# Optimization experiments

Measured on AMD Instinct MI355X. Metric: run time of the kernel, lower is better.

Reference implementation:

```python
import jax, jax.numpy as jnp
import numpy as np

B, P, S = 128, 10, 8
L, BF = 81, 75
OF, MF2 = 40, 20
C = 64
H = 3 * C  # hidden_size = 192
NCHAR = 8
EPS = 1e-5


def setup_inputs() -> dict:
    key = jax.random.key(0)
    ks = jax.random.split(key, 24)
    n = lambda i, shp: jax.random.normal(ks[i], shp, jnp.float32)
    w = lambda i, shp: jax.random.normal(ks[i], shp, jnp.float32) * 0.02
    return {
        "board": n(0, (B, P, S, L, BF)),
        "order": n(1, (B, P, S, OF)),
        "message": n(2, (B, P, S, MF2)),
        "other_ind": jax.random.uniform(ks[3], (B, P, 7), jnp.float32),
        "me_ind": jax.random.uniform(ks[4], (B, P, 7), jnp.float32),
        "h0": n(5, (P, B, H)),
        "c0": n(6, (P, B, H)),
        "Wb1": w(7, (1024, L * BF)), "bb1": jnp.zeros((1024,), jnp.float32),
        "Wb2": w(8, (256, 1024)), "bb2": jnp.zeros((256,), jnp.float32),
        "Wb3": w(9, (C, 256)), "bb3": jnp.zeros((C,), jnp.float32),
        "Wo1": w(10, (128, OF)), "bo1": jnp.zeros((128,), jnp.float32),
        "Wo2": w(11, (32, 128)), "bo2": jnp.zeros((32,), jnp.float32),
        "Wo3": w(12, (C, 32)), "bo3": jnp.zeros((C,), jnp.float32),
        "Wm1": w(13, (64, MF2)), "bm1": jnp.zeros((64,), jnp.float32),
        "Wm2": w(14, (32, 64)), "bm2": jnp.zeros((32,), jnp.float32),
        "Wm3": w(15, (C, 32)), "bm3": jnp.zeros((C,), jnp.float32),
        "g1": jnp.ones((C,), jnp.float32), "be1": jnp.zeros((C,), jnp.float32),
        "g2": jnp.ones((C,), jnp.float32), "be2": jnp.zeros((C,), jnp.float32),
        "g3": jnp.ones((C,), jnp.float32), "be3": jnp.zeros((C,), jnp.float32),
        "Wih": w(16, (4 * H, H)), "Whh": w(17, (4 * H, H)),
        "bih": jnp.zeros((4 * H,), jnp.float32), "bhh": jnp.zeros((4 * H,), jnp.float32),
        "Wf1": w(18, (256, S * H)), "bf1": jnp.zeros((256,), jnp.float32),
        "Wf2": w(19, (NCHAR, 256 + 14)), "bf2": jnp.zeros((NCHAR,), jnp.float32),
    }


def _mlp3(x, W1, b1, W2, b2, W3, b3):
    x = jax.nn.relu(x @ W1.T + b1)
    x = jax.nn.relu(x @ W2.T + b2)
    return x @ W3.T + b3


def _bn_relu(x, g, b):
    # x: [b, C, S]; BatchNorm1d in training mode -> biased batch stats over (N, L)
    m = x.mean(axis=(0, 2), keepdims=True)
    v = jnp.mean((x - m) ** 2, axis=(0, 2), keepdims=True)
    return jax.nn.relu(g[None, :, None] * (x - m) * jax.lax.rsqrt(v + EPS) + b[None, :, None])


def _forward(board, order, message, other_ind, me_ind, h0, c0,
             Wb1, bb1, Wb2, bb2, Wb3, bb3, Wo1, bo1, Wo2, bo2, Wo3, bo3,
             Wm1, bm1, Wm2, bm2, Wm3, bm3, g1, be1, g2, be2, g3, be3,
             Wih, Whh, bih, bhh, Wf1, bf1, Wf2, bf2):
    num_step = board.shape[2]

    def per_past(board_p, order_p, msg_p, oi_p, mi_p, h, c):
        bb = board_p.shape[0]
        bf = _mlp3(board_p.reshape(bb * num_step, -1), Wb1, bb1, Wb2, bb2, Wb3, bb3)
        bf = _bn_relu(jnp.swapaxes(bf.reshape(bb, num_step, -1), 1, 2), g1, be1)
        of = _mlp3(order_p.reshape(bb * num_step, -1), Wo1, bo1, Wo2, bo2, Wo3, bo3)
        of = _bn_relu(jnp.swapaxes(of.reshape(bb, num_step, -1), 1, 2), g2, be2)
        mf = _mlp3(msg_p.reshape(bb * num_step, -1), Wm1, bm1, Wm2, bm2, Wm3, bm3)
        mf = _bn_relu(jnp.swapaxes(mf.reshape(bb, num_step, -1), 1, 2), g3, be3)
        x_feat = jnp.concatenate([bf, of, mf], axis=-1)              # [b, C, 3S]
        x_feat = jnp.transpose(jnp.swapaxes(x_feat, 1, 2), (2, 0, 1))  # [C, b, 3S]
        x_feat = x_feat.reshape(num_step, bb, -1)                    # [S, b, H] (same C-order reindex as torch)

        def step(carry, xt):
            h_, c_ = carry
            gates = xt @ Wih.T + bih + h_ @ Whh.T + bhh
            i, f, g_, o = jnp.split(gates, 4, axis=-1)
            c_ = jax.nn.sigmoid(f) * c_ + jax.nn.sigmoid(i) * jnp.tanh(g_)
            h_ = jax.nn.sigmoid(o) * jnp.tanh(c_)
            return (h_, c_), h_

        _, outs = jax.lax.scan(step, (h, c), x_feat)  # [S, b, H]
        x = jnp.swapaxes(outs, 0, 1).reshape(bb, -1)  # [b, S*H]
        x = jax.nn.relu(x @ Wf1.T + bf1)
        x = jnp.concatenate([x, oi_p, mi_p], axis=-1)  # [b, 256+14]
        return x @ Wf2.T + bf2

    per = jax.vmap(per_past)(
        jnp.swapaxes(board, 0, 1), jnp.swapaxes(order, 0, 1), jnp.swapaxes(message, 0, 1),
        jnp.swapaxes(other_ind, 0, 1), jnp.swapaxes(me_ind, 0, 1), h0, c0)  # [P, b, NCHAR]
    return per.sum(axis=0)


def reference(board, order, message, other_ind, me_ind, h0, c0,
              Wb1, bb1, Wb2, bb2, Wb3, bb3, Wo1, bo1, Wo2, bo2, Wo3, bo3,
              Wm1, bm1, Wm2, bm2, Wm3, bm3, g1, be1, g2, be2, g3, be3,
              Wih, Whh, bih, bhh, Wf1, bf1, Wf2, bf2):
    return _forward(board, order, message, other_ind, me_ind, h0, c0,
                    Wb1, bb1, Wb2, bb2, Wb3, bb3, Wo1, bo1, Wo2, bo2, Wo3, bo3,
                    Wm1, bm1, Wm2, bm2, Wm3, bm3, g1, be1, g2, be2, g3, be3,
                    Wih, Whh, bih, bhh, Wf1, bf1, Wf2, bf2)
```

## Files before the change

### kernel.cpp

```cpp
#include <hip/hip_runtime.h>
#include <stdint.h>

typedef unsigned short u16;
typedef __bf16 v8bf __attribute__((ext_vector_type(8)));
typedef float  v4f  __attribute__((ext_vector_type(4)));

__device__ __forceinline__ u16 f2bf(float f) {
    union { float f; unsigned u; } x; x.f = f;
    unsigned r = (x.u + 0x7FFFu + ((x.u >> 16) & 1u)) >> 16;
    return (u16)r;
}
__device__ __forceinline__ float sigf(float x) { return 1.f / (1.f + __expf(-x)); }
__device__ __forceinline__ void gload(const u16* src, u16* ldst) {
    __builtin_amdgcn_global_load_lds((const __attribute__((address_space(1))) void*)src,
                                     (__attribute__((address_space(3))) void*)ldst, 16, 0, 0);
}

#define OFF_ABF    0UL
#define OFF_XINBF  0UL
#define OFF_XG     3932160UL
#define OFF_FC1    44728320UL
#define OFF_WB1    125829120UL
#define OFF_C1     138412032UL
#define OFF_WB2    159383552UL
#define OFF_WB3    165150720UL
#define OFF_BFE    165216256UL
#define OFF_OFE    167837696UL
#define OFF_MFE    170459136UL
#define OFF_WIH    173095936UL
#define OFF_WHH    173390848UL
#define OFF_WF1    173685760UL
#define OFF_BSUM   174472192UL

__global__ void __launch_bounds__(256) conv_board(const float* __restrict__ src, u16* __restrict__ dst)
{
    int bid = blockIdx.x;
    int row = bid / 6, chunk = bid - row * 6;
    int k0 = chunk * 1024 + threadIdx.x * 4;
    const float* s = src + (long)row * 6075 + k0;
    u16* d = dst + (long)row * 6144 + k0;
    if (k0 + 4 <= 6075) {
        float f0 = s[0], f1 = s[1], f2 = s[2], f3 = s[3];
        uint2 v;
        v.x = (unsigned)f2bf(f0) | ((unsigned)f2bf(f1) << 16);
        v.y = (unsigned)f2bf(f2) | ((unsigned)f2bf(f3) << 16);
        *(uint2*)d = v;
    } else {
#pragma unroll
        for (int z = 0; z < 4; ++z) {
            int k = k0 + z;
            d[z] = f2bf(k < 6075 ? s[z] : 0.f);
        }
    }
}

__global__ void __launch_bounds__(256) conv_weights(
    const float* __restrict__ Wb1, const float* __restrict__ Wb2, const float* __restrict__ Wb3,
    const float* __restrict__ Wih, const float* __restrict__ Whh, const float* __restrict__ Wf1,
    const float* __restrict__ bih, const float* __restrict__ bhh,
    u16* __restrict__ dWb1, u16* __restrict__ dWb2, u16* __restrict__ dWb3,
    u16* __restrict__ dWih, u16* __restrict__ dWhh, u16* __restrict__ dWf1,
    float* __restrict__ bsum)
{
    const long C0 = 6291456, C1 = 6553600, C2 = 6586368, C3 = 6733824,
               C4 = 6881280, C5 = 7274496, C6 = 7275264;
    for (long i = (long)blockIdx.x * 256 + threadIdx.x; i < C6; i += (long)gridDim.x * 256) {
        if (i < C0) {
            int r = (int)(i / 6144), k = (int)(i % 6144);
            dWb1[i] = f2bf(k < 6075 ? Wb1[(long)r * 6075 + k] : 0.f);
        } else if (i < C1) {
            long j = i - C0;
            dWb2[j] = f2bf(Wb2[j]);
        } else if (i < C2) {
            long j = i - C1;
            dWb3[j] = f2bf(j < 16384 ? Wb3[j] : 0.f);
        } else if (i < C3) {
            long j = i - C2;
            dWih[j] = f2bf(Wih[j]);
        } else if (i < C4) {
            long j = i - C3;
            dWhh[j] = f2bf(Whh[j]);
        } else if (i < C5) {
            long j = i - C4;
            dWf1[j] = f2bf(Wf1[j]);
        } else {
            long j = i - C5;
            bsum[j] = bih[j] + bhh[j];
        }
    }
}

#define G160_LDS 73728
__global__ void __launch_bounds__(256, 2)
gemm160(const u16* __restrict__ A, const u16* __restrict__ B,
        const float* __restrict__ bias, u16* __restrict__ C, int K)
{
    extern __shared__ __align__(16) u16 smem[];
    const int tid = threadIdx.x, wv = tid >> 6, lane = tid & 63;
    const int bid = blockIdx.x;
    const int k8 = bid & 7;
    const int j  = bid >> 3;
    const int rowt = k8 + (j >> 3) * 8;
    const int col  = j & 7;
    const long m0 = (long)rowt * 160;
    const long n0 = (long)col * 128;

    const int sr8 = lane >> 3;
    const int sslot = (lane & 7) ^ sr8;
    const u16* Ag = A + (m0 + wv * 8 + sr8) * (long)K + sslot * 8;
    const u16* Bg = B + (n0 + wv * 8 + sr8) * (long)K + sslot * 8;
    const int wr = wv >> 1, wc = wv & 1;
    const int wm = wr * 80, wn = wc * 64;
    const int fr = lane & 15, hi = lane >> 4, fx = fr & 7;

    const int nk = K >> 6;
    v4f acc[5][4] = {};

    auto STAGE = [&](int buf, int t) {
        const long k0 = (long)t * 64;
        const int ab = buf * 18432;
#pragma unroll
        for (int r = 0; r < 5; ++r)
            gload(Ag + (long)r * 32 * K + k0, smem + ab + r * 2048 + wv * 512);
#pragma unroll
        for (int r = 0; r < 4; ++r)
            gload(Bg + (long)r * 32 * K + k0, smem + ab + 10240 + r * 2048 + wv * 512);
    };
    auto LDA_ = [&](int buf, int ks, int i) -> v8bf {
        return *(const v8bf*)(smem + buf * 18432 + (wm + i * 16 + fr) * 64 + ((ks * 4 + hi) ^ fx) * 8);
    };
    auto LDB_ = [&](int buf, int ks, int j2) -> v8bf {
        return *(const v8bf*)(smem + buf * 18432 + 10240 + (wn + j2 * 16 + fr) * 64 + ((ks * 4 + hi) ^ fx) * 8);
    };

    STAGE(0, 0);
    STAGE(1, 1);
    for (int t = 0; t < nk; ++t) {
        const int buf = t & 1;
        if (t + 1 < nk) { asm volatile("s_waitcnt vmcnt(9)" ::: "memory"); }
        else            { asm volatile("s_waitcnt vmcnt(0)" ::: "memory"); }
        asm volatile("s_barrier" ::: "memory");
        __builtin_amdgcn_s_setprio(1);
        v8bf a0[5], a1[5], b0[4], b1[4];
#pragma unroll
        for (int j2 = 0; j2 < 4; ++j2) b0[j2] = LDB_(buf, 0, j2);
#pragma unroll
        for (int i = 0; i < 5; ++i) a0[i] = LDA_(buf, 0, i);
        __builtin_amdgcn_sched_barrier(0);
#pragma unroll
        for (int j2 = 0; j2 < 4; ++j2) b1[j2] = LDB_(buf, 1, j2);
#pragma unroll
        for (int i = 0; i < 5; ++i) a1[i] = LDA_(buf, 1, i);
#pragma unroll
        for (int i = 0; i < 5; ++i)
#pragma unroll
            for (int j2 = 0; j2 < 4; ++j2)
                acc[i][j2] = __builtin_amdgcn_mfma_f32_16x16x32_bf16(a0[i], b0[j2], acc[i][j2], 0, 0, 0);
        __builtin_amdgcn_sched_barrier(0);
        __builtin_amdgcn_s_setprio(0);
        asm volatile("s_waitcnt lgkmcnt(0)" ::: "memory");
        __builtin_amdgcn_sched_barrier(0);
        asm volatile("s_barrier" ::: "memory");
        if (t + 2 < nk) STAGE(buf, t + 2);
        __builtin_amdgcn_s_setprio(1);
#pragma unroll
        for (int i = 0; i < 5; ++i)
#pragma unroll
            for (int j2 = 0; j2 < 4; ++j2)
                acc[i][j2] = __builtin_amdgcn_mfma_f32_16x16x32_bf16(a1[i], b1[j2], acc[i][j2], 0, 0, 0);
        __builtin_amdgcn_s_setprio(0);
    }

#pragma unroll
    for (int i = 0; i < 5; ++i) {
        const long mr = m0 + wm + i * 16 + hi * 4;
#pragma unroll
        for (int j2 = 0; j2 < 4; ++j2) {
            const long n = n0 + wn + j2 * 16 + fr;
            float bv = bias[n];
#pragma unroll
            for (int r = 0; r < 4; ++r) {
                float v = fmaxf(acc[i][j2][r] + bv, 0.f);
                C[(mr + r) * 1024L + n] = f2bf(v);
            }
        }
    }
}

#define L23_LDS 98304
__global__ void __launch_bounds__(512, 1)
gemm_l23(const u16* __restrict__ A, const u16* __restrict__ B, const float* __restrict__ b2,
         const u16* __restrict__ W3, const float* __restrict__ b3, float* __restrict__ Out)
{
    extern __shared__ __align__(16) u16 smem[];
    const int tid = threadIdx.x, wv = tid >> 6, lane = tid & 63;
    const long m0 = (long)blockIdx.x * 128;
    const int sr8 = lane >> 3;
    const int sslot = (lane & 7) ^ sr8;
    const u16* Ag = A + (m0 + wv * 8 + sr8) * 1024L + sslot * 8;
    const u16* Bg = B + (wv * 8 + sr8) * 1024L + sslot * 8;
    const int wr = wv >> 2, wc = wv & 3;
    const int wm = wr * 64, wn = wc * 64;
    const int fr = lane & 15, hi = lane >> 4, fx = fr & 7;

    v4f acc[4][4] = {};

    auto STAGE = [&](int buf, int t) {
        const long k0 = (long)t * 64;
        const int ab = buf * 24576;
#pragma unroll
        for (int r = 0; r < 2; ++r)
            gload(Ag + (long)r * 64 * 1024 + k0, smem + ab + r * 4096 + wv * 512);
#pragma unroll
        for (int r = 0; r < 4; ++r)
            gload(Bg + (long)r * 64 * 1024 + k0, smem + ab + 8192 + r * 4096 + wv * 512);
    };
    auto COMPUTE = [&](int buf) {
#pragma unroll
        for (int ks = 0; ks < 2; ++ks) {
            const int sw = ((ks * 4 + hi) ^ fx) * 8;
            v8bf a[4], b[4];
#pragma unroll
            for (int i = 0; i < 4; ++i)
                a[i] = *(const v8bf*)(smem + buf * 24576 + (wm + i * 16 + fr) * 64 + sw);
#pragma unroll
            for (int j = 0; j < 4; ++j)
                b[j] = *(const v8bf*)(smem + buf * 24576 + 8192 + (wn + j * 16 + fr) * 64 + sw);
#pragma unroll
            for (int i = 0; i < 4; ++i)
#pragma unroll
                for (int j = 0; j < 4; ++j)
                    acc[i][j] = __builtin_amdgcn_mfma_f32_16x16x32_bf16(a[i], b[j], acc[i][j], 0, 0, 0);
        }
    };

    STAGE(0, 0);
    __syncthreads();
    int t = 1;
    while (true) {
        if (t < 16) STAGE(1, t);
        COMPUTE(0);
        if (t >= 16) break;
        __syncthreads();
        ++t;
        if (t < 16) STAGE(0, t);
        COMPUTE(1);
        if (t >= 16) break;
        __syncthreads();
        ++t;
    }
    __syncthreads();
    u16* C2s = smem;
#pragma unroll
    for (int i = 0; i < 4; ++i) {
        const int rrow = wm + i * 16 + hi * 4;
#pragma unroll
        for (int j = 0; j < 4; ++j) {
            const int ccol = wn + j * 16 + fr;
            float bv = b2[ccol];
#pragma unroll
            for (int r = 0; r < 4; ++r)
                C2s[(rrow + r) * 264 + ccol] = f2bf(fmaxf(acc[i][j][r] + bv, 0.f));
        }
    }
    __syncthreads();
    v4f a3[4] = {};
#pragma unroll
    for (int kk = 0; kk < 8; ++kk) {
        v8bf af = *(const v8bf*)(&C2s[(wv * 16 + fr) * 264 + kk * 32 + hi * 8]);
#pragma unroll
        for (int j = 0; j < 4; ++j) {
            v8bf bfr = *(const v8bf*)(W3 + (j * 16 + fr) * 256 + kk * 32 + hi * 8);
            a3[j] = __builtin_amdgcn_mfma_f32_16x16x32_bf16(af, bfr, a3[j], 0, 0, 0);
        }
    }
#pragma unroll
    for (int j = 0; j < 4; ++j) {
        int n = j * 16 + fr;
        float bv = b3[n];
#pragma unroll
        for (int q = 0; q < 4; ++q)
            Out[(m0 + wv * 16 + hi * 4 + q) * 64 + n] = a3[j][q] + bv;
    }
}

template<int OBF, int RELU, int BIAS>
__global__ void __launch_bounds__(256)
gemm_bt(const u16* __restrict__ A, const u16* __restrict__ B,
        const float* __restrict__ bias, void* __restrict__ Cv,
        int M, int N, int K, int ldc)
{
    __shared__ __align__(16) u16 As[2][128 * 64];
    __shared__ __align__(16) u16 Bs[2][128 * 64];
    const int tid = threadIdx.x;
    const int wv = tid >> 6, lane = tid & 63;
    const long m0 = (long)blockIdx.y * 128;
    const long n0 = (long)blockIdx.x * 128;
    const int srow  = wv * 8 + (lane >> 3);
    const int sslot = (lane & 7) ^ (lane >> 3);
    const u16* Ag = A + (m0 + srow) * (long)K + sslot * 8;
    const u16* Bg = B + (n0 + srow) * (long)K + sslot * 8;
    const int wm = (wv >> 1) * 64, wn = (wv & 1) * 64;
    const int fr = lane & 15, hi = lane >> 4;
    const int fx = fr & 7;

    v4f acc[4][4] = {};
    const int nk = K >> 6;

    auto STAGE = [&](int buf, int k0) {
#pragma unroll
        for (int r = 0; r < 4; ++r)
            gload(Ag + (long)r * 32 * K + k0, &As[buf][r * 2048 + wv * 512]);
#pragma unroll
        for (int r = 0; r < 4; ++r)
            gload(Bg + (long)r * 32 * K + k0, &Bs[buf][r * 2048 + wv * 512]);
    };
    auto COMPUTE = [&](int buf) {
#pragma unroll
        for (int ks = 0; ks < 2; ++ks) {
            v8bf a[4], b[4];
            const int sw = (((ks * 4 + hi) ^ fx)) * 8;
#pragma unroll
            for (int i = 0; i < 4; ++i)
                a[i] = *(const v8bf*)(&As[buf][(wm + i * 16 + fr) * 64 + sw]);
#pragma unroll
            for (int j = 0; j < 4; ++j)
                b[j] = *(const v8bf*)(&Bs[buf][(wn + j * 16 + fr) * 64 + sw]);
#pragma unroll
            for (int i = 0; i < 4; ++i)
#pragma unroll
                for (int j = 0; j < 4; ++j)
                    acc[i][j] = __builtin_amdgcn_mfma_f32_16x16x32_bf16(a[i], b[j], acc[i][j], 0, 0, 0);
        }
    };

    STAGE(0, 0);
    __syncthreads();
    int t = 1;
    while (true) {
        if (t < nk) STAGE(1, t * 64);
        COMPUTE(0);
        if (t >= nk) break;
        __syncthreads();
        ++t;
        if (t < nk) STAGE(0, t * 64);
        COMPUTE(1);
        if (t >= nk) break;
        __syncthreads();
        ++t;
    }

#pragma unroll
    for (int i = 0; i < 4; ++i) {
        const long mr = m0 + wm + i * 16 + hi * 4;
#pragma unroll
        for (int j = 0; j < 4; ++j) {
            const long n = n0 + wn + j * 16 + fr;
            if (n < N) {
                float bv = BIAS ? bias[n] : 0.f;
#pragma unroll
                for (int r = 0; r < 4; ++r) {
                    float v = acc[i][j][r] + bv;
                    if (RELU) v = fmaxf(v, 0.f);
                    if (OBF) ((u16*)Cv)[(mr + r) * (long)ldc + n] = f2bf(v);
                    else     ((float*)Cv)[(mr + r) * (long)ldc + n] = v;
                }
            }
        }
    }
}

template<int D0, int D1>
__device__ __forceinline__ void mlp3_body(
    float* sm, const float* __restrict__ X,
    const float* __restrict__ W1, const float* __restrict__ B1,
    const float* __restrict__ W2, const float* __restrict__ B2,
    const float* __restrict__ W3, const float* __restrict__ B3,
    float* __restrict__ Out, int blk)
{
    float* w1s = sm;
    float* w2s = w1s + D0 * D1;
    float* w3s = w2s + D1 * 32;
    float* b1s = w3s + 32 * 64;
    float* b2s = b1s + D1;
    float* b3s = b2s + 32;
    float* xs  = b3s + 64;
    float* h1  = xs + 32 * D0;
    float* h2  = h1 + 32 * D1;

    const int tid = threadIdx.x;
    const long row0 = (long)blk * 32;

    for (int i = tid; i < D0 * D1; i += 256) { int k = i / D1, n = i % D1; w1s[i] = W1[n * D0 + k]; }
    for (int i = tid; i < D1 * 32; i += 256) { int k = i / 32,  n = i % 32; w2s[i] = W2[n * D1 + k]; }
    for (int i = tid; i < 32 * 64; i += 256) { int k = i / 64,  n = i % 64; w3s[i] = W3[n * 32 + k]; }
    if (tid < D1) b1s[tid] = B1[tid];
    if (tid < 32) b2s[tid] = B2[tid];
    if (tid < 64) b3s[tid] = B3[tid];
    for (int i = tid; i < 32 * D0; i += 256) xs[i] = X[(row0 + i / D0) * D0 + i % D0];
    __syncthreads();

    const int wv = tid >> 6, lane = tid & 63;
    const int r0 = wv * 8;
    {
        constexpr int NL = D1 / 64;
        float acc[NL][8];
#pragma unroll
        for (int a = 0; a < NL; ++a)
#pragma unroll
            for (int r = 0; r < 8; ++r) acc[a][r] = 0.f;
        for (int k = 0; k < D0; ++k) {
            float w[NL];
#pragma unroll
            for (int a = 0; a < NL; ++a) w[a] = w1s[k * D1 + lane + a * 64];
#pragma unroll
            for (int r = 0; r < 8; ++r) {
                float x = xs[(r0 + r) * D0 + k];
#pragma unroll
                for (int a = 0; a < NL; ++a) acc[a][r] += w[a] * x;
            }
        }
#pragma unroll
        for (int a = 0; a < NL; ++a)
#pragma unroll
            for (int r = 0; r < 8; ++r)
                h1[(r0 + r) * D1 + lane + a * 64] = fmaxf(acc[a][r] + b1s[lane + a * 64], 0.f);
    }
    __syncthreads();
    {
        int n = lane & 31;
        int rb = r0 + (lane >> 5) * 4;
        float acc[4] = {0, 0, 0, 0};
        for (int k = 0; k < D1; ++k) {
            float w = w2s[k * 32 + n];
#pragma unroll
            for (int r = 0; r < 4; ++r) acc[r] += w * h1[(rb + r) * D1 + k];
        }
#pragma unroll
        for (int r = 0; r < 4; ++r) h2[(rb + r) * 32 + n] = fmaxf(acc[r] + b2s[n], 0.f);
    }
    __syncthreads();
    {
        float acc[8] = {};
        for (int k = 0; k < 32; ++k) {
            float w = w3s[k * 64 + lane];
#pragma unroll
            for (int r = 0; r < 8; ++r) acc[r] += w * h2[(r0 + r) * 32 + k];
        }
#pragma unroll
        for (int r = 0; r < 8; ++r) Out[(row0 + r0 + r) * 64 + lane] = acc[r] + b3s[lane];
    }
}

#define MLP_LDS 71552
__global__ void __launch_bounds__(256)
mlp3_dual(const float* __restrict__ Xo,
          const float* __restrict__ Wo1, const float* __restrict__ bo1,
          const float* __restrict__ Wo2, const float* __restrict__ bo2,
          const float* __restrict__ Wo3, const float* __restrict__ bo3,
          float* __restrict__ ofe,
          const float* __restrict__ Xm,
          const float* __restrict__ Wm1, const float* __restrict__ bm1,
          const float* __restrict__ Wm2, const float* __restrict__ bm2,
          const float* __restrict__ Wm3, const float* __restrict__ bm3,
          float* __restrict__ mfe)
{
    extern __shared__ __align__(16) float sm[];
    if (blockIdx.x < 320)
        mlp3_body<40, 128>(sm, Xo, Wo1, bo1, Wo2, bo2, Wo3, bo3, ofe, blockIdx.x);
    else
        mlp3_body<20, 64>(sm, Xm, Wm1, bm1, Wm2, bm2, Wm3, bm3, mfe, blockIdx.x - 320);
}

#define BX_LDS 100032
__global__ void __launch_bounds__(256, 1)
build_xin2(const float* __restrict__ bfe, const float* __restrict__ ofe, const float* __restrict__ mfe,
           const float* __restrict__ g1, const float* __restrict__ be1,
           const float* __restrict__ g2, const float* __restrict__ be2,
           const float* __restrict__ g3, const float* __restrict__ be3,
           u16* __restrict__ xin)
{
    extern __shared__ __align__(16) float ls[];
    float* coefA = ls + 24576;
    float* coefB = coefA + 24;
    float* psum  = coefB + 24;
    float* psum2 = psum + 192;
    const int p = blockIdx.x >> 3, s = blockIdx.x & 7;
    const int tid = threadIdx.x;
    const float* Fs[3] = {bfe, ofe, mfe};
    for (int g = tid; g < 3072; g += 256) {
        int br = g >> 10, rr = g & 1023, bb = rr >> 3, tt = rr & 7;
        const float* srcp = Fs[br] + ((long)(bb * 80 + p * 8 + tt)) * 64 + s * 8;
        float4 v0 = *(const float4*)srcp;
        float4 v1 = *(const float4*)(srcp + 4);
        *(float4*)(ls + (long)g * 8) = v0;
        *(float4*)(ls + (long)g * 8 + 4) = v1;
    }
    __syncthreads();
    if (tid < 192) {
        int pair = tid >> 3, part = tid & 7;
        int br = pair >> 3, cl = pair & 7;
        float s1 = 0.f, s2 = 0.f;
        for (int b2 = 0; b2 < 16; ++b2) {
            int bb = part * 16 + b2;
            const float* base = ls + ((br * 128 + bb) * 8) * 8 + cl;
#pragma unroll
            for (int tt = 0; tt < 8; ++tt) { float v = base[tt * 8]; s1 += v; s2 += v * v; }
        }
        psum[tid] = s1; psum2[tid] = s2;
    }
    __syncthreads();
    if (tid < 24) {
        float s1 = 0.f, s2 = 0.f;
#pragma unroll
        for (int q = 0; q < 8; ++q) { s1 += psum[tid * 8 + q]; s2 += psum2[tid * 8 + q]; }
        int br = tid >> 3, cl = tid & 7, c = s * 8 + cl;
        const float* G  = br == 0 ? g1  : (br == 1 ? g2  : g3);
        const float* BE = br == 0 ? be1 : (br == 1 ? be2 : be3);
        float m  = s1 * (1.f / 1024.f);
        float var = s2 * (1.f / 1024.f) - m * m;
        float Aa = G[c] * rsqrtf(var + 1e-5f);
        coefA[tid] = Aa;
        coefB[tid] = BE[c] - Aa * m;
    }
    __syncthreads();
    const int u = tid >> 1, h0 = (tid & 1) * 96;
    const long obase = ((long)(p * 8 + s) * 128 + u) * 192 + h0;
    const int cl = u >> 4;
    const int ub = (u & 15) * 8;
    union { u16 u[8]; uint4 v; } pk;
    for (int hq = 0; hq < 12; ++hq) {
#pragma unroll
        for (int z = 0; z < 8; ++z) {
            int h = h0 + hq * 8 + z;
            int bb = ub + h / 24, t = h % 24, br = t >> 3, tt = t & 7;
            float v = ls[((br * 128 + bb) * 8 + tt) * 8 + cl];
            float r = fmaxf(v * coefA[br * 8 + cl] + coefB[br * 8 + cl], 0.f);
            pk.u[z] = f2bf(r);
        }
        *(uint4*)(xin + obase + hq * 8) = pk.v;
    }
}

#define LSTM_LDS (6400 + 49152)
__global__ void __launch_bounds__(512, 1)
lstm_persist(const float* __restrict__ Xg, const u16* __restrict__ Whh,
             const float* __restrict__ h0, const float* __restrict__ c0,
             const u16* __restrict__ Wf1, const float* __restrict__ bf1,
             float* __restrict__ fc1o)
{
    extern __shared__ __align__(16) u16 smem[];
    u16*   hS    = smem;
    float* gates = (float*)(smem + 16 * 200);

    const int tid = threadIdx.x, wv = tid >> 6, lane = tid & 63;
    const int R0 = blockIdx.x * 16;
    const int fr = lane & 15, hi = lane >> 4;

    v8bf Wreg[6][6];
#pragma unroll
    for (int nt = 0; nt < 6; ++nt)
#pragma unroll
        for (int ks = 0; ks < 6; ++ks)
            Wreg[nt][ks] = *(const v8bf*)(Whh + (long)(nt * 128 + wv * 16 + fr) * 192 + ks * 32 + hi * 8);

    for (int i = tid; i < 16 * 200; i += 512) {
        int r = i / 200, cx = i % 200;
        hS[i] = (cx < 192) ? f2bf(h0[(R0 + r) * 192 + cx]) : (u16)0;
    }
    float creg[6];
#pragma unroll
    for (int j = 0; j < 6; ++j) {
        int e = j * 512 + tid;
        creg[j] = c0[(R0 + e / 192) * 192 + e % 192];
    }

    v4f f1acc[2] = {};
    const int nb0 = wv * 32;
    auto WF1ACC = [&](int ss, const v8bf* a) {
#pragma unroll
        for (int jf = 0; jf < 2; ++jf) {
            v4f tacc = f1acc[jf];
#pragma unroll
            for (int ks = 0; ks < 6; ++ks) {
                v8bf bfr = *(const v8bf*)(Wf1 + (long)(nb0 + jf * 16 + fr) * 1536 + ss * 192 + ks * 32 + hi * 8);
                tacc = __builtin_amdgcn_mfma_f32_16x16x32_bf16(a[ks], bfr, tacc, 0, 0, 0);
            }
            f1acc[jf] = tacc;
        }
    };

    for (int s = 0; s < 8; ++s) {
        __syncthreads();
        v8bf a[6];
#pragma unroll
        for (int ks = 0; ks < 6; ++ks)
            a[ks] = *(const v8bf*)(&hS[fr * 200 + ks * 32 + hi * 8]);
        if (s > 0) WF1ACC(s - 1, a);
#pragma unroll
        for (int nt = 0; nt < 6; ++nt) {
            v4f acc = {};
#pragma unroll
            for (int ks = 0; ks < 6; ++ks)
                acc = __builtin_amdgcn_mfma_f32_16x16x32_bf16(a[ks], Wreg[nt][ks], acc, 0, 0, 0);
            int n = nt * 128 + wv * 16 + fr;
#pragma unroll
            for (int q = 0; q < 4; ++q)
                gates[(hi * 4 + q) * 768 + n] = acc[q];
        }
        __syncthreads();
#pragma unroll
        for (int j = 0; j < 6; ++j) {
            int e = j * 512 + tid;
            int r = e / 192, hd = e % 192;
            int grow = R0 + r;
            int p = grow >> 7, u = grow & 127;
            long xrow = (long)((p * 8 + s) * 128 + u) * 768;
            float gi = Xg[xrow + hd]       + gates[r * 768 + hd];
            float gf = Xg[xrow + 192 + hd] + gates[r * 768 + 192 + hd];
            float gg = Xg[xrow + 384 + hd] + gates[r * 768 + 384 + hd];
            float go = Xg[xrow + 576 + hd] + gates[r * 768 + 576 + hd];
            float c = sigf(gf) * creg[j] + sigf(gi) * tanhf(gg);
            float h = sigf(go) * tanhf(c);
            creg[j] = c;
            hS[r * 200 + hd] = f2bf(h);
        }
    }
    __syncthreads();
    {
        v8bf a[6];
#pragma unroll
        for (int ks = 0; ks < 6; ++ks)
            a[ks] = *(const v8bf*)(&hS[fr * 200 + ks * 32 + hi * 8]);
        WF1ACC(7, a);
    }
#pragma unroll
    for (int jf = 0; jf < 2; ++jf)
#pragma unroll
        for (int q = 0; q < 4; ++q) {
            int row = hi * 4 + q;
            int n = nb0 + jf * 16 + fr;
            fc1o[(long)(R0 + row) * 256 + n] = fmaxf(f1acc[jf][q] + bf1[n], 0.f);
        }
}

__global__ void __launch_bounds__(256) final_fc2(
    const float* __restrict__ fc1, const float* __restrict__ oi, const float* __restrict__ mi,
    const float* __restrict__ Wf2, const float* __restrict__ bf2, float* __restrict__ out)
{
    const int wv = threadIdx.x >> 6, lane = threadIdx.x & 63;
    const int w = blockIdx.x * 4 + wv;
    const int u = w >> 3, n = w & 7;
    const float* wrow = Wf2 + n * 270;
    float wreg[4];
#pragma unroll
    for (int q = 0; q < 4; ++q) wreg[q] = wrow[lane + 64 * q];
    float wtail = (lane < 14) ? wrow[256 + lane] : 0.f;
    float acc = 0.f;
    for (int p = 0; p < 10; ++p) {
        const float* x = fc1 + (long)(p * 128 + u) * 256;
#pragma unroll
        for (int q = 0; q < 4; ++q) acc += x[lane + 64 * q] * wreg[q];
        float t = 0.f;
        if (lane < 7)       t = oi[(u * 10 + p) * 7 + lane];
        else if (lane < 14) t = mi[(u * 10 + p) * 7 + lane - 7];
        acc += t * wtail;
    }
#pragma unroll
    for (int off = 32; off; off >>= 1) acc += __shfl_xor(acc, off);
    if (lane == 0) out[u * 8 + n] = acc + bf2[n];
}

extern "C" void kernel_launch(void* const* d_in, const int* in_sizes, int n_in,
                              void* d_out, int out_size, void* d_ws, size_t ws_size,
                              hipStream_t stream)
{
    (void)in_sizes; (void)n_in; (void)out_size; (void)ws_size;
    const float* board = (const float*)d_in[0];
    const float* order = (const float*)d_in[1];
    const float* mess  = (const float*)d_in[2];
    const float* oi    = (const float*)d_in[3];
    const float* mi    = (const float*)d_in[4];
    const float* h0    = (const float*)d_in[5];
    const float* c0    = (const float*)d_in[6];
    const float* Wb1 = (const float*)d_in[7];  const float* bb1 = (const float*)d_in[8];
    const float* Wb2 = (const float*)d_in[9];  const float* bb2 = (const float*)d_in[10];
    const float* Wb3 = (const float*)d_in[11]; const float* bb3 = (const float*)d_in[12];
    const float* Wo1 = (const float*)d_in[13]; const float* bo1 = (const float*)d_in[14];
    const float* Wo2 = (const float*)d_in[15]; const float* bo2 = (const float*)d_in[16];
    const float* Wo3 = (const float*)d_in[17]; const float* bo3 = (const float*)d_in[18];
    const float* Wm1 = (const float*)d_in[19]; const float* bm1 = (const float*)d_in[20];
    const float* Wm2 = (const float*)d_in[21]; const float* bm2 = (const float*)d_in[22];
    const float* Wm3 = (const float*)d_in[23]; const float* bm3 = (const float*)d_in[24];
    const float* g1  = (const float*)d_in[25]; const float* be1 = (const float*)d_in[26];
    const float* g2  = (const float*)d_in[27]; const float* be2 = (const float*)d_in[28];
    const float* g3  = (const float*)d_in[29]; const float* be3 = (const float*)d_in[30];
    const float* Wih = (const float*)d_in[31]; const float* Whh = (const float*)d_in[32];
    const float* bih = (const float*)d_in[33]; const float* bhh = (const float*)d_in[34];
    const float* Wf1 = (const float*)d_in[35]; const float* bf1 = (const float*)d_in[36];
    const float* Wf2 = (const float*)d_in[37]; const float* bf2 = (const float*)d_in[38];

    uint8_t* ws = (uint8_t*)d_ws;
    u16*   A_bf    = (u16*)(ws + OFF_ABF);
    u16*   xin_bf  = (u16*)(ws + OFF_XINBF);
    float* Xg      = (float*)(ws + OFF_XG);
    float* fc1o    = (float*)(ws + OFF_FC1);
    u16*   Wb1_bf  = (u16*)(ws + OFF_WB1);
    u16*   C1_bf   = (u16*)(ws + OFF_C1);
    u16*   Wb2_bf  = (u16*)(ws + OFF_WB2);
    u16*   Wb3_bf  = (u16*)(ws + OFF_WB3);
    float* bfe     = (float*)(ws + OFF_BFE);
    float* ofe     = (float*)(ws + OFF_OFE);
    float* mfe     = (float*)(ws + OFF_MFE);
    u16*   Wih_bf  = (u16*)(ws + OFF_WIH);
    u16*   Whh_bf  = (u16*)(ws + OFF_WHH);
    u16*   Wf1_bf  = (u16*)(ws + OFF_WF1);
    float* bsum    = (float*)(ws + OFF_BSUM);

    conv_board<<<61440, 256, 0, stream>>>(board, A_bf);
    conv_weights<<<2048, 256, 0, stream>>>(Wb1, Wb2, Wb3, Wih, Whh, Wf1, bih, bhh,
                                           Wb1_bf, Wb2_bf, Wb3_bf, Wih_bf, Whh_bf, Wf1_bf, bsum);

    hipFuncSetAttribute(reinterpret_cast<const void*>(gemm160),
                        hipFuncAttributeMaxDynamicSharedMemorySize, G160_LDS);
    gemm160<<<512, 256, G160_LDS, stream>>>(A_bf, Wb1_bf, bb1, C1_bf, 6144);
    hipFuncSetAttribute(reinterpret_cast<const void*>(gemm_l23),
                        hipFuncAttributeMaxDynamicSharedMemorySize, L23_LDS);
    gemm_l23<<<80, 512, L23_LDS, stream>>>(C1_bf, Wb2_bf, bb2, Wb3_bf, bb3, bfe);

    hipFuncSetAttribute(reinterpret_cast<const void*>(mlp3_dual),
                        hipFuncAttributeMaxDynamicSharedMemorySize, MLP_LDS);
    mlp3_dual<<<640, 256, MLP_LDS, stream>>>(order, Wo1, bo1, Wo2, bo2, Wo3, bo3, ofe,
                                             mess, Wm1, bm1, Wm2, bm2, Wm3, bm3, mfe);

    hipFuncSetAttribute(reinterpret_cast<const void*>(build_xin2),
                        hipFuncAttributeMaxDynamicSharedMemorySize, BX_LDS);
    build_xin2<<<80, 256, BX_LDS, stream>>>(bfe, ofe, mfe, g1, be1, g2, be2, g3, be3, xin_bf);

    gemm_bt<0, 0, 1><<<dim3(6, 80), 256, 0, stream>>>(xin_bf, Wih_bf, bsum, Xg, 10240, 768, 192, 768);

    hipFuncSetAttribute(reinterpret_cast<const void*>(lstm_persist),
                        hipFuncAttributeMaxDynamicSharedMemorySize, LSTM_LDS);
    lstm_persist<<<80, 512, LSTM_LDS, stream>>>(Xg, Whh_bf, h0, c0, Wf1_bf, bf1, fc1o);

    final_fc2<<<256, 256, 0, stream>>>(fc1o, oi, mi, Wf2, bf2, (float*)d_out);
}
```

Baseline: 375.1 us.

## Fuse board fp32-to-bf16 conversion into the first GEMM's A-tile loading

Drops the separate conv_board kernel. The first board GEMM now reads the fp32 board directly into registers, converts it to bf16, and writes the swizzled tile into LDS. This removes a full write and re-read of a ~250MB-scale intermediate and one kernel launch. The cost is register-staged A loads (40 floats per thread) that replace async global-to-LDS loads, which may raise register pressure and make latency harder to hide at two blocks per CU. The fp32 A tile is read uncoalesced at row stride 6075, with boundary handling on the last tile.

```diff
diff --git a/kernel.cpp b/kernel.cpp
--- a/kernel.cpp
+++ b/kernel.cpp
@@ -10,13 +10,15 @@
     unsigned r = (x.u + 0x7FFFu + ((x.u >> 16) & 1u)) >> 16;
     return (u16)r;
 }
+__device__ __forceinline__ unsigned pkbf(float a, float b) {
+    return (unsigned)f2bf(a) | ((unsigned)f2bf(b) << 16);
+}
 __device__ __forceinline__ float sigf(float x) { return 1.f / (1.f + __expf(-x)); }
 __device__ __forceinline__ void gload(const u16* src, u16* ldst) {
     __builtin_amdgcn_global_load_lds((const __attribute__((address_space(1))) void*)src,
                                      (__attribute__((address_space(3))) void*)ldst, 16, 0, 0);
 }
 
-#define OFF_ABF    0UL
 #define OFF_XINBF  0UL
 #define OFF_XG     3932160UL
 #define OFF_FC1    44728320UL
@@ -31,28 +33,6 @@
 #define OFF_WHH    173390848UL
 #define OFF_WF1    173685760UL
 #define OFF_BSUM   174472192UL
-
-__global__ void __launch_bounds__(256) conv_board(const float* __restrict__ src, u16* __restrict__ dst)
-{
-    int bid = blockIdx.x;
-    int row = bid / 6, chunk = bid - row * 6;
-    int k0 = chunk * 1024 + threadIdx.x * 4;
-    const float* s = src + (long)row * 6075 + k0;
-    u16* d = dst + (long)row * 6144 + k0;
-    if (k0 + 4 <= 6075) {
-        float f0 = s[0], f1 = s[1], f2 = s[2], f3 = s[3];
-        uint2 v;
-        v.x = (unsigned)f2bf(f0) | ((unsigned)f2bf(f1) << 16);
-        v.y = (unsigned)f2bf(f2) | ((unsigned)f2bf(f3) << 16);
-        *(uint2*)d = v;
-    } else {
-#pragma unroll
-        for (int z = 0; z < 4; ++z) {
-            int k = k0 + z;
-            d[z] = f2bf(k < 6075 ? s[z] : 0.f);
-        }
-    }
-}
 
 __global__ void __launch_bounds__(256) conv_weights(
     const float* __restrict__ Wb1, const float* __restrict__ Wb2, const float* __restrict__ Wb3,
@@ -92,8 +72,8 @@
 
 #define G160_LDS 73728
 __global__ void __launch_bounds__(256, 2)
-gemm160(const u16* __restrict__ A, const u16* __restrict__ B,
-        const float* __restrict__ bias, u16* __restrict__ C, int K)
+gemm160f(const float* __restrict__ A32, const u16* __restrict__ B,
+         const float* __restrict__ bias, u16* __restrict__ C, int K)
 {
     extern __shared__ __align__(16) u16 smem[];
     const int tid = threadIdx.x, wv = tid >> 6, lane = tid & 63;
@@ -107,24 +87,59 @@
 
     const int sr8 = lane >> 3;
     const int sslot = (lane & 7) ^ sr8;
-    const u16* Ag = A + (m0 + wv * 8 + sr8) * (long)K + sslot * 8;
     const u16* Bg = B + (n0 + wv * 8 + sr8) * (long)K + sslot * 8;
     const int wr = wv >> 1, wc = wv & 1;
     const int wm = wr * 80, wn = wc * 64;
     const int fr = lane & 15, hi = lane >> 4, fx = fr & 7;
 
     const int nk = K >> 6;
-    v4f acc[5][4] = {};
-
-    auto STAGE = [&](int buf, int t) {
+
+    const int arow0 = tid >> 4;
+    const int col4  = tid & 15;
+    const float* pa[10];
+#pragma unroll
+    for (int q = 0; q < 10; ++q)
+        pa[q] = A32 + (m0 + q * 16 + arow0) * 6075L + col4 * 4;
+    const int awbase = arow0 * 64 + (((col4 >> 1) ^ (arow0 & 7)) * 8) + (col4 & 1) * 4;
+
+    float R[40];
+    auto AL = [&](int tile) {
+        if (tile < 94) {
+#pragma unroll
+            for (int q = 0; q < 10; ++q) {
+#pragma unroll
+                for (int jj = 0; jj < 4; ++jj) R[q * 4 + jj] = pa[q][jj];
+                pa[q] += 64;
+            }
+        } else {
+            int kb = tile * 64 + col4 * 4;
+#pragma unroll
+            for (int q = 0; q < 10; ++q) {
+#pragma unroll
+                for (int jj = 0; jj < 4; ++jj) {
+                    float v = 0.f;
+                    if (kb + jj < 6075) v = pa[q][jj];
+                    R[q * 4 + jj] = v;
+                }
+                pa[q] += 64;
+            }
+        }
+    };
+    auto AWRITE = [&](int bufofs) {
+#pragma unroll
+        for (int q = 0; q < 10; ++q) {
+            uint2 w;
+            w.x = pkbf(R[q * 4 + 0], R[q * 4 + 1]);
+            w.y = pkbf(R[q * 4 + 2], R[q * 4 + 3]);
+            *(uint2*)(smem + bufofs + awbase + q * 1024) = w;
+        }
+    };
+    auto SB = [&](int buf, int t) {
         const long k0 = (long)t * 64;
-        const int ab = buf * 18432;
-#pragma unroll
-        for (int r = 0; r < 5; ++r)
-            gload(Ag + (long)r * 32 * K + k0, smem + ab + r * 2048 + wv * 512);
+        const int ab = buf * 18432 + 10240;
 #pragma unroll
         for (int r = 0; r < 4; ++r)
-            gload(Bg + (long)r * 32 * K + k0, smem + ab + 10240 + r * 2048 + wv * 512);
+            gload(Bg + (long)r * 32 * K + k0, smem + ab + r * 2048 + wv * 512);
     };
     auto LDA_ = [&](int buf, int ks, int i) -> v8bf {
         return *(const v8bf*)(smem + buf * 18432 + (wm + i * 16 + fr) * 64 + ((ks * 4 + hi) ^ fx) * 8);
@@ -133,13 +148,20 @@
         return *(const v8bf*)(smem + buf * 18432 + 10240 + (wn + j2 * 16 + fr) * 64 + ((ks * 4 + hi) ^ fx) * 8);
     };
 
-    STAGE(0, 0);
-    STAGE(1, 1);
+    v4f acc[5][4] = {};
+
+    SB(0, 0);
+    SB(1, 1);
+    AL(0);
+    asm volatile("s_waitcnt vmcnt(8)" ::: "memory");
+    AWRITE(0);
+
     for (int t = 0; t < nk; ++t) {
         const int buf = t & 1;
-        if (t + 1 < nk) { asm volatile("s_waitcnt vmcnt(9)" ::: "memory"); }
-        else            { asm volatile("s_waitcnt vmcnt(0)" ::: "memory"); }
+        asm volatile("s_waitcnt vmcnt(4) lgkmcnt(0)" ::: "memory");
         asm volatile("s_barrier" ::: "memory");
+        if (t + 1 < nk) AL(t + 1);
+        __builtin_amdgcn_sched_barrier(0);
         __builtin_amdgcn_s_setprio(1);
         v8bf a0[5], a1[5], b0[4], b1[4];
 #pragma unroll
@@ -161,7 +183,13 @@
         asm volatile("s_waitcnt lgkmcnt(0)" ::: "memory");
         __builtin_amdgcn_sched_barrier(0);
         asm volatile("s_barrier" ::: "memory");
-        if (t + 2 < nk) STAGE(buf, t + 2);
+        if (t + 2 < nk) SB(buf, t + 2);
+        if (t + 1 < nk) {
+            if (t + 2 < nk) { asm volatile("s_waitcnt vmcnt(4)" ::: "memory"); }
+            else            { asm volatile("s_waitcnt vmcnt(0)" ::: "memory"); }
+            AWRITE((buf ^ 1) * 18432);
+        }
+        __builtin_amdgcn_sched_barrier(0);
         __builtin_amdgcn_s_setprio(1);
 #pragma unroll
         for (int i = 0; i < 5; ++i)
@@ -701,7 +729,6 @@
     const float* Wf2 = (const float*)d_in[37]; const float* bf2 = (const float*)d_in[38];
 
     uint8_t* ws = (uint8_t*)d_ws;
-    u16*   A_bf    = (u16*)(ws + OFF_ABF);
     u16*   xin_bf  = (u16*)(ws + OFF_XINBF);
     float* Xg      = (float*)(ws + OFF_XG);
     float* fc1o    = (float*)(ws + OFF_FC1);
@@ -717,13 +744,12 @@
     u16*   Wf1_bf  = (u16*)(ws + OFF_WF1);
     float* bsum    = (float*)(ws + OFF_BSUM);
 
-    conv_board<<<61440, 256, 0, stream>>>(board, A_bf);
     conv_weights<<<2048, 256, 0, stream>>>(Wb1, Wb2, Wb3, Wih, Whh, Wf1, bih, bhh,
                                            Wb1_bf, Wb2_bf, Wb3_bf, Wih_bf, Whh_bf, Wf1_bf, bsum);
 
-    hipFuncSetAttribute(reinterpret_cast<const void*>(gemm160),
+    hipFuncSetAttribute(reinterpret_cast<const void*>(gemm160f),
                         hipFuncAttributeMaxDynamicSharedMemorySize, G160_LDS);
-    gemm160<<<512, 256, G160_LDS, stream>>>(A_bf, Wb1_bf, bb1, C1_bf, 6144);
+    gemm160f<<<512, 256, G160_LDS, stream>>>(board, Wb1_bf, bb1, C1_bf, 6144);
     hipFuncSetAttribute(reinterpret_cast<const void*>(gemm_l23),
                         hipFuncAttributeMaxDynamicSharedMemorySize, L23_LDS);
     gemm_l23<<<80, 512, L23_LDS, stream>>>(C1_bf, Wb2_bf, bb2, Wb3_bf, bb3, bfe);
```

New measurement: 441.2 us. 1.18x slower.
